# Kernel optimization log

Hardware: AMD Instinct MI355X
Metric: run time of the kernel (lower is better)

The kernel has to match this reference:

```python
import jax, jax.numpy as jnp
import numpy as np

N_NODES = 100000
N_EDGES = 3200000
IN_FEATS = 128
H_FEATS = 256
REG_NUM = 1


def _linear_params(key, fan_in, fan_out):
    kw, kb = jax.random.split(key)
    bound = 1.0 / np.sqrt(fan_in)
    W = jax.random.uniform(kw, (fan_out, fan_in), minval=-bound, maxval=bound, dtype=jnp.float32)
    b = jax.random.uniform(kb, (fan_out,), minval=-bound, maxval=bound, dtype=jnp.float32)
    return W, b


def setup_inputs() -> dict:
    key = jax.random.key(0)
    ks = jax.random.split(key, 12)
    node_feat = jax.random.normal(ks[0], (N_NODES, IN_FEATS), dtype=jnp.float32)
    edge_feat = jax.random.normal(ks[1], (N_EDGES, 1), dtype=jnp.float32)
    edge_dst = jax.random.randint(ks[2], (N_EDGES,), 0, N_NODES, dtype=jnp.int64)
    # SAGE layer weights: conv1 maps in_feats+1 -> h_feats; mids map h_feats+1 -> h_feats
    W1, b1 = _linear_params(ks[3], IN_FEATS + 1, H_FEATS)
    Wm1, bm1 = _linear_params(ks[4], H_FEATS + 1, H_FEATS)
    Wm2, bm2 = _linear_params(ks[5], H_FEATS + 1, H_FEATS)
    Wm3, bm3 = _linear_params(ks[6], H_FEATS + 1, H_FEATS)
    Wm4, bm4 = _linear_params(ks[7], H_FEATS + 1, H_FEATS)
    Wr1, br1 = _linear_params(ks[8], H_FEATS + 1, H_FEATS)
    Wr2, br2 = _linear_params(ks[9], H_FEATS, H_FEATS)
    Wr3, br3 = _linear_params(ks[10], H_FEATS, REG_NUM)
    return {
        "node_feat": node_feat, "edge_feat": edge_feat, "edge_dst": edge_dst,
        "W1": W1, "b1": b1,
        "Wm1": Wm1, "bm1": bm1, "Wm2": Wm2, "bm2": bm2,
        "Wm3": Wm3, "bm3": bm3, "Wm4": Wm4, "bm4": bm4,
        "Wr1": Wr1, "br1": br1, "Wr2": Wr2, "br2": br2, "Wr3": Wr3, "br3": br3,
    }


def _sage_layer(hn, he_aggr, W, b):
    # concat [N, d] with [N, 1] then linear
    h_total = jnp.concatenate([hn, he_aggr], axis=1)
    return h_total @ W.T + b


def reference(node_feat, edge_feat, edge_dst,
              W1, b1, Wm1, bm1, Wm2, bm2, Wm3, bm3, Wm4, bm4,
              Wr1, br1, Wr2, br2, Wr3, br3):
    # copy_e + sum: scatter-add edge features onto destination nodes -> [N, 1]
    he_aggr = jax.ops.segment_sum(edge_feat, edge_dst, num_segments=N_NODES)
    h = jax.nn.relu(_sage_layer(node_feat, he_aggr, W1, b1))  # dropout = identity (eval)
    h = jax.nn.relu(_sage_layer(h, he_aggr, Wm1, bm1))
    h = jax.nn.relu(_sage_layer(h, he_aggr, Wm2, bm2))
    h = jax.nn.relu(_sage_layer(h, he_aggr, Wm3, bm3))
    h = jax.nn.relu(_sage_layer(h, he_aggr, Wm4, bm4))
    h = jax.nn.relu(_sage_layer(h, he_aggr, Wr1, br1))
    h = jax.nn.relu(h @ Wr2.T + br2)
    return h @ Wr3.T + br3
```

## Files before the change

kernel.cpp:

```cpp
#include <hip/hip_runtime.h>
#include <hip/hip_bf16.h>

typedef _Float16 half8  __attribute__((ext_vector_type(8)));
typedef _Float16 half4v __attribute__((ext_vector_type(4)));
typedef float    f32x4  __attribute__((ext_vector_type(4)));

#define N_NODES 100000
#define N_EDGES 3200000
#define SH_STRIDE 100096
#define NBUCK 782
#define CAP   5120
#define CHUNK 4096
#define NBIN  782
#define NPK   32

__global__ __launch_bounds__(512) void binpack(
    const float* __restrict__ ef, const int* __restrict__ dst,
    const float* __restrict__ W1,  const float* __restrict__ Wm1,
    const float* __restrict__ Wm2, const float* __restrict__ Wm3,
    const float* __restrict__ Wm4, const float* __restrict__ Wr1,
    const float* __restrict__ Wr2,
    const float* __restrict__ b1,  const float* __restrict__ bm1,
    const float* __restrict__ bm2, const float* __restrict__ bm3,
    const float* __restrict__ bm4, const float* __restrict__ br1,
    const float* __restrict__ br2, const float* __restrict__ wr3,
    const float* __restrict__ br3,
    int* __restrict__ cursor, unsigned* __restrict__ pairs,
    _Float16* __restrict__ Wp, float* __restrict__ park, int do_bin) {

    if (do_bin && blockIdx.x < NBIN) {
        __shared__ int      hist[NBUCK];
        __shared__ int      base[NBUCK];
        __shared__ int      lbase[NBUCK];
        __shared__ int      wsum[8];
        __shared__ unsigned lrec[CHUNK];
        __shared__ int      lslot[CHUNK];
        const int start = blockIdx.x * CHUNK;
        const int tid   = threadIdx.x;
        const int wave  = tid >> 6;
        const int lane  = tid & 63;
        for (int b = tid; b < NBUCK; b += 512) hist[b] = 0;
        __syncthreads();

        int4   dreg[2];
        float4 freg[2];
        int    rnk[2][4];
        #pragma unroll
        for (int it = 0; it < 2; ++it) {
            const int i = start + (it * 512 + tid) * 4;
            if (i < N_EDGES) {
                dreg[it] = *(const int4*)&dst[i];
                freg[it] = *(const float4*)&ef[i];
                rnk[it][0] = atomicAdd(&hist[dreg[it].x >> 7], 1);
                rnk[it][1] = atomicAdd(&hist[dreg[it].y >> 7], 1);
                rnk[it][2] = atomicAdd(&hist[dreg[it].z >> 7], 1);
                rnk[it][3] = atomicAdd(&hist[dreg[it].w >> 7], 1);
            }
        }
        __syncthreads();

        for (int b = tid; b < NBUCK; b += 512) {
            const int c = hist[b];
            base[b] = b * CAP + ((c > 0) ? atomicAdd(&cursor[b], c) : 0);
        }
        const int b0 = 2 * tid, b1 = 2 * tid + 1;
        const int h0 = (b0 < NBUCK) ? hist[b0] : 0;
        const int h1 = (b1 < NBUCK) ? hist[b1] : 0;
        const int psum = h0 + h1;
        int pfx = psum;
        #pragma unroll
        for (int ofs = 1; ofs < 64; ofs <<= 1) {
            const int v = __shfl_up(pfx, ofs);
            if (lane >= ofs) pfx += v;
        }
        if (lane == 63) wsum[wave] = pfx;
        __syncthreads();
        int woff = 0;
        #pragma unroll
        for (int w = 0; w < 8; ++w) woff += (w < wave) ? wsum[w] : 0;
        const int excl = woff + pfx - psum;
        if (b0 < NBUCK) lbase[b0] = excl;
        if (b1 < NBUCK) lbase[b1] = excl + h0;
        __syncthreads();

        #pragma unroll
        for (int it = 0; it < 2; ++it) {
            const int i = start + (it * 512 + tid) * 4;
            if (i < N_EDGES) {
                const int4   d = dreg[it];
                const float4 f = freg[it];
                {   const int bk = d.x >> 7; const int r = rnk[it][0];
                    const int s = lbase[bk] + r; const int g = base[bk] + r;
                    lrec[s]  = (__float_as_uint(f.x) & 0xFFFFFF00u) | (unsigned)(d.x & 127);
                    lslot[s] = (g < (bk + 1) * CAP) ? g : -1; }
                {   const int bk = d.y >> 7; const int r = rnk[it][1];
                    const int s = lbase[bk] + r; const int g = base[bk] + r;
                    lrec[s]  = (__float_as_uint(f.y) & 0xFFFFFF00u) | (unsigned)(d.y & 127);
                    lslot[s] = (g < (bk + 1) * CAP) ? g : -1; }
                {   const int bk = d.z >> 7; const int r = rnk[it][2];
                    const int s = lbase[bk] + r; const int g = base[bk] + r;
                    lrec[s]  = (__float_as_uint(f.z) & 0xFFFFFF00u) | (unsigned)(d.z & 127);
                    lslot[s] = (g < (bk + 1) * CAP) ? g : -1; }
                {   const int bk = d.w >> 7; const int r = rnk[it][3];
                    const int s = lbase[bk] + r; const int g = base[bk] + r;
                    lrec[s]  = (__float_as_uint(f.w) & 0xFFFFFF00u) | (unsigned)(d.w & 127);
                    lslot[s] = (g < (bk + 1) * CAP) ? g : -1; }
            }
        }
        __syncthreads();
        const int total = min(CHUNK, N_EDGES - start);
        for (int s = tid; s < total; s += 512) {
            const int g = lslot[s];
            if (g >= 0) pairs[g] = lrec[s];
        }
    } else {
        const float* srcs[7] = {W1, Wm1, Wm2, Wm3, Wm4, Wr1, Wr2};
        const float* bias[7] = {b1, bm1, bm2, bm3, bm4, br1, br2};
        const int pb  = do_bin ? ((int)blockIdx.x - NBIN) : (int)blockIdx.x;
        const int gid = pb * 512 + threadIdx.x;
        const int gsz = NPK * 512;
        for (int i = gid; i < 425984; i += gsz) {
            int job, w, s, j, lane, e, stride;
            if (i < 32768) {
                job = 0; stride = 129;
                w = i >> 13;
                const int rem = i & 8191;
                s = rem >> 11;
                j = (rem >> 9) & 3;
                lane = (rem >> 3) & 63;
                e = rem & 7;
            } else {
                const int t = i - 32768;
                job = 1 + (t >> 16);
                const int local = t & 65535;
                stride = (job == 6) ? 256 : 257;
                w = local >> 14;
                const int rem = local & 16383;
                s = rem >> 11;
                j = (rem >> 9) & 3;
                lane = (rem >> 3) & 63;
                e = rem & 7;
            }
            const int row = w * 64 + j * 16 + (lane & 15);
            const int col = s * 32 + ((lane >> 4) << 3) + e;
            Wp[i] = (_Float16)srcs[job][row * stride + col];
        }
        for (int i = gid; i < 1536; i += gsz) {
            const int job = i >> 8, row = i & 255;
            const int stride = (job == 0) ? 129 : 257;
            const int kin    = (job == 0) ? 128 : 256;
            park[job * 512 + row] = srcs[job][row * stride + kin];
        }
        for (int i = gid; i < 256; i += gsz) park[6 * 512 + i] = 0.f;
        for (int i = gid; i < 1792; i += gsz)
            park[(i >> 8) * 512 + 256 + (i & 255)] = bias[i >> 8][i & 255];
        for (int i = gid; i < 256; i += gsz) park[3584 + i] = wr3[i];
        if (gid == 0) park[3840] = br3[0];
    }
}

__global__ void scatter4(const float4* __restrict__ ef4,
                         const int4* __restrict__ dst4,
                         float* __restrict__ e) {
    const int n4 = N_EDGES / 4;
    for (int i = blockIdx.x * blockDim.x + threadIdx.x; i < n4;
         i += gridDim.x * blockDim.x) {
        const float4 f = ef4[i];
        const int4   d = dst4[i];
        atomicAdd(&e[d.x], f.x);
        atomicAdd(&e[SH_STRIDE + d.y], f.y);
        atomicAdd(&e[2 * SH_STRIDE + d.z], f.z);
        atomicAdd(&e[3 * SH_STRIDE + d.w], f.w);
    }
}

template<int K>
__device__ __forceinline__ void layer_mm(const _Float16* __restrict__ Wl,
                                         _Float16 (* __restrict__ Hs)[264],
                                         const float* __restrict__ es,
                                         const float* __restrict__ parkl,
                                         int wave, int lane, int m_, int quad) {
    f32x4 acc[4][8];
    #pragma unroll
    for (int jt = 0; jt < 4; ++jt)
        #pragma unroll
        for (int mt = 0; mt < 8; ++mt)
            acc[jt][mt] = (f32x4){0.f, 0.f, 0.f, 0.f};

    const int jb0 = wave * 64 + quad * 4;
    float4 w4[4], bb[4];
    #pragma unroll
    for (int jt = 0; jt < 4; ++jt) {
        w4[jt] = *(const float4*)&parkl[jt * 16 + jb0];
        bb[jt] = *(const float4*)&parkl[256 + jt * 16 + jb0];
    }

    const _Float16* __restrict__ wp = Wl + (size_t)wave * (64 * K) + lane * 8;

    half8 a[4];
    #pragma unroll
    for (int jt = 0; jt < 4; ++jt)
        a[jt] = *(const half8*)(wp + jt * 512);

    half8 b[8];
    #pragma unroll
    for (int mt = 0; mt < 8; ++mt)
        b[mt] = *(const half8*)&Hs[mt * 16 + m_][quad * 8];

    #pragma unroll
    for (int kk = 0; kk < K; kk += 32) {
        const int s = kk >> 5;
        half8 a2[4];
        if (kk + 32 < K) {
            #pragma unroll
            for (int jt = 0; jt < 4; ++jt)
                a2[jt] = *(const half8*)(wp + ((s + 1) * 4 + jt) * 512);
        }
        #pragma unroll
        for (int mt = 0; mt < 8; ++mt) {
            #pragma unroll
            for (int jt = 0; jt < 4; ++jt)
                acc[jt][mt] = __builtin_amdgcn_mfma_f32_16x16x32_f16(
                    a[jt], b[mt], acc[jt][mt], 0, 0, 0);
            if (kk + 32 < K)
                b[mt] = *(const half8*)&Hs[mt * 16 + m_][kk + 32 + quad * 8];
        }
        if (kk + 32 < K) {
            #pragma unroll
            for (int jt = 0; jt < 4; ++jt) a[jt] = a2[jt];
        }
    }
    __syncthreads();

    #pragma unroll
    for (int jt = 0; jt < 4; ++jt) {
        const int jbase = jb0 + jt * 16;
        #pragma unroll
        for (int mt = 0; mt < 8; ++mt) {
            const int node = mt * 16 + m_;
            const float ev = es[node];
            half4v h;
            h[0] = (_Float16)fmaxf(acc[jt][mt][0] + ev * w4[jt].x + bb[jt].x, 0.f);
            h[1] = (_Float16)fmaxf(acc[jt][mt][1] + ev * w4[jt].y + bb[jt].y, 0.f);
            h[2] = (_Float16)fmaxf(acc[jt][mt][2] + ev * w4[jt].z + bb[jt].z, 0.f);
            h[3] = (_Float16)fmaxf(acc[jt][mt][3] + ev * w4[jt].w + bb[jt].w, 0.f);
            *(half4v*)&Hs[node][jbase] = h;
        }
    }
    __syncthreads();
}

__global__ __launch_bounds__(256, 2) void sage_fused(
    const float* __restrict__ node_feat,
    const int* __restrict__ cursor, const unsigned* __restrict__ pairs,
    const float* __restrict__ esh, int nsh,
    const _Float16* __restrict__ Wpack, const float* __restrict__ park,
    float* __restrict__ out) {

    __shared__ _Float16 Hs[128][264];
    __shared__ float esp[528];
    __shared__ float es[128];
    __shared__ float wf[256];
    __shared__ float red[2][128];

    const int tid  = threadIdx.x;
    const int wave = tid >> 6;
    const int lane = tid & 63;
    const int m_   = lane & 15;
    const int quad = lane >> 4;
    const int node0 = blockIdx.x * 128;

    for (int i = tid; i < 528; i += 256) esp[i] = 0.f;

    int cnt = 0;
    if (nsh == 0) cnt = min(cursor[blockIdx.x], CAP);
    __syncthreads();

    for (int idx = tid; idx < 128 * 16; idx += 256) {
        const int row = idx >> 4, g = idx & 15;
        int node = node0 + row; if (node >= N_NODES) node = N_NODES - 1;
        const float4* src = (const float4*)(node_feat + (size_t)node * 128 + g * 8);
        const float4 v0 = src[0], v1 = src[1];
        half8 h;
        h[0] = (_Float16)v0.x; h[1] = (_Float16)v0.y;
        h[2] = (_Float16)v0.z; h[3] = (_Float16)v0.w;
        h[4] = (_Float16)v1.x; h[5] = (_Float16)v1.y;
        h[6] = (_Float16)v1.z; h[7] = (_Float16)v1.w;
        *(half8*)&Hs[row][g * 8] = h;
    }
    if (nsh == 0) {
        const unsigned* __restrict__ pp = pairs + (size_t)blockIdx.x * CAP;
        const int sh = (tid & 3) * 132;
        for (int i = tid; i < cnt; i += 256) {
            const unsigned p = pp[i];
            atomicAdd(&esp[sh + (p & 127u)], __uint_as_float(p & 0xFFFFFF00u));
        }
    } else if (tid < 128) {
        int node = node0 + tid; if (node >= N_NODES) node = N_NODES - 1;
        float s = 0.f;
        for (int sh = 0; sh < nsh; ++sh) s += esh[(size_t)sh * SH_STRIDE + node];
        esp[tid] = s;
    }
    __syncthreads();
    if (tid < 128)
        es[tid] = esp[tid] + esp[132 + tid] + esp[264 + tid] + esp[396 + tid];
    __syncthreads();

    layer_mm<128>(Wpack, Hs, es, park, wave, lane, m_, quad);
    for (int l = 1; l < 7; ++l)
        layer_mm<256>(Wpack + 32768 + (l - 1) * 65536, Hs, es, park + l * 512,
                      wave, lane, m_, quad);

    wf[tid] = park[3584 + tid];
    __syncthreads();
    {
        const int row = tid & 127, seg = tid >> 7;
        const _Float16* hp = &Hs[row][seg * 128];
        const float* wpt = &wf[seg * 128];
        float s = 0.f;
        #pragma unroll
        for (int k = 0; k < 16; ++k) {
            const half8 h = *(const half8*)(hp + k * 8);
            const float* w8 = wpt + k * 8;
            s += (float)h[0] * w8[0] + (float)h[1] * w8[1]
               + (float)h[2] * w8[2] + (float)h[3] * w8[3]
               + (float)h[4] * w8[4] + (float)h[5] * w8[5]
               + (float)h[6] * w8[6] + (float)h[7] * w8[7];
        }
        red[seg][row] = s;
    }
    __syncthreads();
    if (tid < 128) {
        const int node = node0 + tid;
        if (node < N_NODES)
            out[node] = red[0][tid] + red[1][tid] + park[3840];
    }
}

extern "C" void kernel_launch(void* const* d_in, const int* in_sizes, int n_in,
                              void* d_out, int out_size, void* d_ws,
                              size_t ws_size, hipStream_t stream) {
    const float* node_feat = (const float*)d_in[0];
    const float* edge_feat = (const float*)d_in[1];
    const int*   edge_dst  = (const int*)d_in[2];
    const float* W1  = (const float*)d_in[3];  const float* b1  = (const float*)d_in[4];
    const float* Wm1 = (const float*)d_in[5];  const float* bm1 = (const float*)d_in[6];
    const float* Wm2 = (const float*)d_in[7];  const float* bm2 = (const float*)d_in[8];
    const float* Wm3 = (const float*)d_in[9];  const float* bm3 = (const float*)d_in[10];
    const float* Wm4 = (const float*)d_in[11]; const float* bm4 = (const float*)d_in[12];
    const float* Wr1 = (const float*)d_in[13]; const float* br1 = (const float*)d_in[14];
    const float* Wr2 = (const float*)d_in[15]; const float* br2 = (const float*)d_in[16];
    const float* Wr3 = (const float*)d_in[17]; const float* br3 = (const float*)d_in[18];
    float* out = (float*)d_out;

    char* ws = (char*)d_ws;
    int*      cursor = (int*)ws;
    _Float16* Wp     = (_Float16*)(ws + 4096);
    float*    park   = (float*)(ws + 856064);
    unsigned* pairs  = (unsigned*)(ws + 872448);
    float*    esh    = (float*)(ws + 872448);

    const size_t need_bins = 872448 + (size_t)NBUCK * CAP * 4;
    const bool use_bins = (ws_size >= need_bins);

    const int nblk = (N_NODES + 127) / 128;

    if (use_bins) {
        hipMemsetAsync(cursor, 0, NBUCK * sizeof(int), stream);
        binpack<<<NBIN + NPK, 512, 0, stream>>>(
            edge_feat, edge_dst, W1, Wm1, Wm2, Wm3, Wm4, Wr1, Wr2,
            b1, bm1, bm2, bm3, bm4, br1, br2, Wr3, br3,
            cursor, pairs, Wp, park, 1);
        sage_fused<<<nblk, 256, 0, stream>>>(node_feat, cursor, pairs,
                                             nullptr, 0, Wp, park, out);
    } else {
        binpack<<<NPK, 512, 0, stream>>>(
            edge_feat, edge_dst, W1, Wm1, Wm2, Wm3, Wm4, Wr1, Wr2,
            b1, bm1, bm2, bm3, bm4, br1, br2, Wr3, br3,
            cursor, pairs, Wp, park, 0);
        hipMemsetAsync(esh, 0, (size_t)4 * SH_STRIDE * 4, stream);
        scatter4<<<3125, 256, 0, stream>>>((const float4*)edge_feat,
                                           (const int4*)edge_dst, esh);
        sage_fused<<<nblk, 256, 0, stream>>>(node_feat, nullptr, nullptr,
                                             esh, 4, Wp, park, out);
    }
}
```

Baseline: 277.6 us.

## Interleave edge-sum atomics with first layer MFMA loop

The first layer's matmul is inlined, and the per-block edge scatter-add atomics into shared memory are split into four slices placed between the K-steps of the MFMA loop. The edge sum is reduced only after the matmul finishes and is then applied in the epilogue. The aim is to hide shared-memory atomic latency behind tensor-core work rather than serialize it before layer one. In exchange the code is longer and register pressure rises, since the accumulators live across the atomic loop.

```diff
diff --git a/kernel.cpp b/kernel.cpp
--- a/kernel.cpp
+++ b/kernel.cpp
@@ -288,25 +288,97 @@
         h[6] = (_Float16)v1.z; h[7] = (_Float16)v1.w;
         *(half8*)&Hs[row][g * 8] = h;
     }
-    if (nsh == 0) {
-        const unsigned* __restrict__ pp = pairs + (size_t)blockIdx.x * CAP;
-        const int sh = (tid & 3) * 132;
-        for (int i = tid; i < cnt; i += 256) {
-            const unsigned p = pp[i];
-            atomicAdd(&esp[sh + (p & 127u)], __uint_as_float(p & 0xFFFFFF00u));
-        }
-    } else if (tid < 128) {
+    if (nsh != 0 && tid < 128) {
         int node = node0 + tid; if (node >= N_NODES) node = N_NODES - 1;
         float s = 0.f;
         for (int sh = 0; sh < nsh; ++sh) s += esh[(size_t)sh * SH_STRIDE + node];
         esp[tid] = s;
     }
     __syncthreads();
-    if (tid < 128)
-        es[tid] = esp[tid] + esp[132 + tid] + esp[264 + tid] + esp[396 + tid];
-    __syncthreads();
-
-    layer_mm<128>(Wpack, Hs, es, park, wave, lane, m_, quad);
+
+    {
+        f32x4 acc[4][8];
+        #pragma unroll
+        for (int jt = 0; jt < 4; ++jt)
+            #pragma unroll
+            for (int mt = 0; mt < 8; ++mt)
+                acc[jt][mt] = (f32x4){0.f, 0.f, 0.f, 0.f};
+
+        const int jb0 = wave * 64 + quad * 4;
+        float4 w4[4], bb4[4];
+        #pragma unroll
+        for (int jt = 0; jt < 4; ++jt) {
+            w4[jt]  = *(const float4*)&park[jt * 16 + jb0];
+            bb4[jt] = *(const float4*)&park[256 + jt * 16 + jb0];
+        }
+
+        const _Float16* __restrict__ wp =
+            Wpack + (size_t)wave * (64 * 128) + lane * 8;
+        half8 a[4];
+        #pragma unroll
+        for (int jt = 0; jt < 4; ++jt)
+            a[jt] = *(const half8*)(wp + jt * 512);
+        half8 b[8];
+        #pragma unroll
+        for (int mt = 0; mt < 8; ++mt)
+            b[mt] = *(const half8*)&Hs[mt * 16 + m_][quad * 8];
+
+        const unsigned* __restrict__ pp = pairs + (size_t)blockIdx.x * CAP;
+        const int sh = (tid & 3) * 132;
+
+        #pragma unroll
+        for (int kk = 0; kk < 128; kk += 32) {
+            const int s = kk >> 5;
+            half8 a2[4];
+            if (kk + 32 < 128) {
+                #pragma unroll
+                for (int jt = 0; jt < 4; ++jt)
+                    a2[jt] = *(const half8*)(wp + ((s + 1) * 4 + jt) * 512);
+            }
+            if (nsh == 0) {
+                for (int i = tid + (s << 8); i < cnt; i += 1024) {
+                    const unsigned p = pp[i];
+                    atomicAdd(&esp[sh + (p & 127u)],
+                              __uint_as_float(p & 0xFFFFFF00u));
+                }
+            }
+            #pragma unroll
+            for (int mt = 0; mt < 8; ++mt) {
+                #pragma unroll
+                for (int jt = 0; jt < 4; ++jt)
+                    acc[jt][mt] = __builtin_amdgcn_mfma_f32_16x16x32_f16(
+                        a[jt], b[mt], acc[jt][mt], 0, 0, 0);
+                if (kk + 32 < 128)
+                    b[mt] = *(const half8*)&Hs[mt * 16 + m_][kk + 32 + quad * 8];
+            }
+            if (kk + 32 < 128) {
+                #pragma unroll
+                for (int jt = 0; jt < 4; ++jt) a[jt] = a2[jt];
+            }
+        }
+        __syncthreads();
+        if (tid < 128)
+            es[tid] = esp[tid] + esp[132 + tid] + esp[264 + tid] + esp[396 + tid];
+        __syncthreads();
+
+        #pragma unroll
+        for (int jt = 0; jt < 4; ++jt) {
+            const int jbase = jb0 + jt * 16;
+            #pragma unroll
+            for (int mt = 0; mt < 8; ++mt) {
+                const int node = mt * 16 + m_;
+                const float ev = es[node];
+                half4v h;
+                h[0] = (_Float16)fmaxf(acc[jt][mt][0] + ev * w4[jt].x + bb4[jt].x, 0.f);
+                h[1] = (_Float16)fmaxf(acc[jt][mt][1] + ev * w4[jt].y + bb4[jt].y, 0.f);
+                h[2] = (_Float16)fmaxf(acc[jt][mt][2] + ev * w4[jt].z + bb4[jt].z, 0.f);
+                h[3] = (_Float16)fmaxf(acc[jt][mt][3] + ev * w4[jt].w + bb4[jt].w, 0.f);
+                *(half4v*)&Hs[node][jbase] = h;
+            }
+        }
+        __syncthreads();
+    }
+
     for (int l = 1; l < 7; ++l)
         layer_mm<256>(Wpack + 32768 + (l - 1) * 65536, Hs, es, park + l * 512,
                       wave, lane, m_, quad);
```

New measurement: 277.4 us. No clear change (-0.1%).
